# Optimization experiments

Measured on AMD Instinct MI355X. Metric: run time of the kernel, lower is better.

Reference implementation:

```python
import jax, jax.numpy as jnp
import numpy as np

NGRAM = 4
PAD = 0
N_LAYERS = sum(range(1, NGRAM + 1)) - 1  # 9; blocks_size = 10


def setup_inputs() -> dict:
    B, L, D, V = 8, 2048, 256, 256
    rng = np.random.default_rng(0)
    lens = rng.integers(L // 2, L + 1, size=B)
    pos = np.arange(L)
    seq = rng.integers(1, V, size=(B, L))
    seq = np.where(pos[None, :] < lens[:, None], seq, PAD)
    # per-layer block sizes: (size,offset) combos of GBST, sizes [2,2,3,3,3,4,4,4,4]
    sizes = [n for n in range(1, NGRAM + 1) for _ in range(n)][1:]
    gid = np.zeros((B, N_LAYERS, L), dtype=np.int64)
    for li, s in enumerate(sizes):
        g = pos // s + 1  # sorted contiguous group ids starting at 1
        gid[:, li, :] = np.where(pos[None, :] < lens[:, None], g[None, :], PAD)

    key = jax.random.key(0)
    ks = jax.random.split(key, 8)
    emb = jax.random.normal(ks[0], (V, D), jnp.float32) * 0.02
    conv_w = jax.random.normal(ks[1], (D, 1, NGRAM), jnp.float32) * 0.3      # depthwise Conv1d weight [out,1,k]
    conv_b = jax.random.normal(ks[2], (D,), jnp.float32) * 0.01
    proj_w = jax.random.normal(ks[3], (D, D), jnp.float32) / np.sqrt(D)      # 1x1 conv as [out,in]
    proj_b = jax.random.normal(ks[4], (D,), jnp.float32) * 0.01
    score_w = jax.random.normal(ks[5], (D,), jnp.float32) / np.sqrt(D)       # Linear(D,1)
    score_b = jnp.zeros((), jnp.float32)
    ff_w = jax.random.normal(ks[6], (D, D), jnp.float32) / np.sqrt(D)        # Linear(D,D) weight [out,in]
    ff_b = jax.random.normal(ks[7], (D,), jnp.float32) * 0.01
    return {
        "sequence": jnp.asarray(seq, jnp.int64) if jax.config.jax_enable_x64 else jnp.asarray(seq, jnp.int32),
        "group_id": jnp.asarray(gid, jnp.int64) if jax.config.jax_enable_x64 else jnp.asarray(gid, jnp.int32),
        "emb": emb, "conv_w": conv_w, "conv_b": conv_b,
        "proj_w": proj_w, "proj_b": proj_b,
        "score_w": score_w, "score_b": score_b,
        "ff_w": ff_w, "ff_b": ff_b,
    }


def _pool_one(xb, gb):
    """Per-(batch,layer) scatter_mean + broadcast back. xb:[L,D], gb:[L]."""
    L = gb.shape[0]
    mask = gb == PAD
    xm = jnp.where(mask[:, None], 0.0, xb)          # zero padded positions
    pad_g = jnp.max(gb) + 1                         # pad positions -> extra trailing group
    g = jnp.where(mask, pad_g, gb) - 1              # 0-based group ids
    sums = jax.ops.segment_sum(xm, g, num_segments=L)
    cnts = jax.ops.segment_sum(jnp.ones((L,), xb.dtype), g, num_segments=L)
    means = sums / jnp.maximum(cnts, 1.0)[:, None]
    # group ids are sorted-contiguous, so repeat_interleave(bincount) == gather
    return means[g]


def reference(sequence, group_id, emb, conv_w, conv_b, proj_w, proj_b,
              score_w, score_b, ff_w, ff_b):
    B, L = sequence.shape
    D = emb.shape[1]
    # NormalizedEmbedding: lookup * sqrt(d_model)
    x = emb[sequence] * jnp.sqrt(jnp.asarray(D, emb.dtype))          # [B,L,D]
    xp = jnp.pad(x, ((0, 0), (0, NGRAM - 1), (0, 0)))                # pad seq end
    xc = xp.transpose(0, 2, 1)                                       # [B,D,L+k-1]
    xc = jax.lax.conv_general_dilated(
        xc, conv_w, window_strides=(1,), padding='VALID',
        feature_group_count=D, dimension_numbers=('NCH', 'OIH', 'NCH'))
    xc = xc + conv_b[None, :, None]
    xc = jnp.einsum('ed,bdl->bel', proj_w, xc) + proj_b[None, :, None]
    x = xc.transpose(0, 2, 1)                                        # [B,L,D]
    seq_mask = sequence == PAD
    x = jnp.where(seq_mask[..., None], 0.0, x)

    # layers 1..9 are computed on a detached copy in the original
    xd = jax.lax.stop_gradient(x)
    pooled = jax.vmap(jax.vmap(_pool_one, in_axes=(None, 0)),
                      in_axes=(0, 0))(xd, group_id)                  # [B,9,L,D]

    block_reps = jnp.concatenate([x[:, None], pooled], axis=1)       # [B,10,L,D]
    block_reps = block_reps.transpose(0, 2, 1, 3)                    # [B,L,10,D]

    scores = jnp.einsum('blsd,d->bls', block_reps, score_w) + score_b
    blocks_mask = jnp.concatenate([sequence[:, None], group_id], axis=1)
    blocks_mask = blocks_mask.transpose(0, 2, 1) == PAD              # [B,L,10]
    neg = -jnp.finfo(scores.dtype).max
    scores = jnp.where(blocks_mask, neg, scores)
    scores = jax.nn.softmax(scores, axis=2)

    out = jnp.einsum('blsd,bls->bld', block_reps, scores)            # [B,L,D]
    out = out + jax.nn.relu(out @ ff_w.T + ff_b)
    return out
```

## Files before the change

kernel.cpp:

```cpp
#include <hip/hip_runtime.h>
#include <math.h>


#define D_ 256
#define M_ 24
#define BPB 86
#define LSTR 264

typedef __attribute__((ext_vector_type(8))) short bf16x8;
typedef __attribute__((ext_vector_type(4))) float f32x4;

__device__ __forceinline__ ushort f2bf(float f) {
    union { float f; unsigned u; } v; v.f = f;
    unsigned r = v.u + 0x7fffu + ((v.u >> 16) & 1u);
    return (ushort)(r >> 16);
}
__device__ __forceinline__ float bf2f(ushort h) {
    union { unsigned u; float f; } v; v.u = ((unsigned)h) << 16;
    return v.f;
}

#define LDB4(v0, v1, v2, v3, W, K8) do { \
    const ushort* bp_ = (W) + ((size_t)((K8) * 16 + w * 4) * 64 + ln) * 8; \
    v0 = *(const bf16x8*)(bp_); \
    v1 = *(const bf16x8*)(bp_ + 512); \
    v2 = *(const bf16x8*)(bp_ + 1024); \
    v3 = *(const bf16x8*)(bp_ + 1536); \
} while (0)

#define MFMA8(ACC, K8, v0, v1, v2, v3) do { \
    bf16x8 a0_ = *(const bf16x8*)&x_lds[lr][(K8) * 32 + koff]; \
    bf16x8 a1_ = *(const bf16x8*)&x_lds[16 + lr][(K8) * 32 + koff]; \
    ACC[0][0] = __builtin_amdgcn_mfma_f32_16x16x32_bf16(a0_, v0, ACC[0][0], 0, 0, 0); \
    ACC[1][0] = __builtin_amdgcn_mfma_f32_16x16x32_bf16(a1_, v0, ACC[1][0], 0, 0, 0); \
    ACC[0][1] = __builtin_amdgcn_mfma_f32_16x16x32_bf16(a0_, v1, ACC[0][1], 0, 0, 0); \
    ACC[1][1] = __builtin_amdgcn_mfma_f32_16x16x32_bf16(a1_, v1, ACC[1][1], 0, 0, 0); \
    ACC[0][2] = __builtin_amdgcn_mfma_f32_16x16x32_bf16(a0_, v2, ACC[0][2], 0, 0, 0); \
    ACC[1][2] = __builtin_amdgcn_mfma_f32_16x16x32_bf16(a1_, v2, ACC[1][2], 0, 0, 0); \
    ACC[0][3] = __builtin_amdgcn_mfma_f32_16x16x32_bf16(a0_, v3, ACC[0][3], 0, 0, 0); \
    ACC[1][3] = __builtin_amdgcn_mfma_f32_16x16x32_bf16(a1_, v3, ACC[1][3], 0, 0, 0); \
} while (0)

#define SBAR __builtin_amdgcn_sched_barrier(0)

__global__ __launch_bounds__(256) void k_prep(
    const float* __restrict__ pw, const float* __restrict__ fw,
    const float* __restrict__ emb,
    ushort* __restrict__ wqp, ushort* __restrict__ wqf, ushort* __restrict__ we)
{
    int i = blockIdx.x * 256 + threadIdx.x;
    we[i] = f2bf(emb[i] * 16.0f);
    int j  = i & 7;
    int ln = (i >> 3) & 63;
    int nb = (i >> 9) & 15;
    int k8 = i >> 13;
    int er = nb * 16 + (ln & 15);
    int k  = k8 * 32 + (ln >> 4) * 8 + j;
    wqp[i] = f2bf(pw[er * D_ + k]);
    wqf[i] = f2bf(fw[er * D_ + k]);
}

__global__ __launch_bounds__(256, 3) void k_main(
    const int* __restrict__ seq, const ushort* __restrict__ we,
    const float* __restrict__ conv_w, const float* __restrict__ conv_b,
    const ushort* __restrict__ wqp, const float* __restrict__ proj_b,
    const float* __restrict__ score_w,
    const ushort* __restrict__ wqf, const float* __restrict__ ff_b,
    float* __restrict__ out, int L)
{
    __shared__ ushort x_lds[32][LSTR];
    __shared__ ushort x2[M_][LSTR];
    __shared__ float xsred[4][M_];
    __shared__ float wts[4][12][4];
    __shared__ int sseq[4][M_ + 3];
    const int b  = blockIdx.x / BPB;
    const int l0 = (blockIdx.x % BPB) * M_;
    const int t  = threadIdx.x;
    const int w  = t >> 6, ln = t & 63;
    const int lr = ln & 15, q = ln >> 4;
    const int koff = q * 8;

    if (ln < M_ + 3) {
        int l = l0 + ln;
        sseq[w][ln] = (l < L) ? seq[b * L + l] : -1;
    }
    {
        int zr = 24 + (t >> 5), zc = (t & 31) * 8;
        *(uint4*)&x_lds[zr][zc] = make_uint4(0, 0, 0, 0);
    }
    bf16x8 s00, s01, s02, s03, s10, s11, s12, s13;
    bf16x8 s20, s21, s22, s23, s30, s31, s32, s33;
    LDB4(s00, s01, s02, s03, wqp, 0);
    LDB4(s10, s11, s12, s13, wqp, 1);
    LDB4(s20, s21, s22, s23, wqp, 2);
    LDB4(s30, s31, s32, s33, wqp, 3);
    SBAR;
    asm volatile("s_waitcnt lgkmcnt(0)" ::: "memory");
    SBAR;

    {
        const int h = t >> 7;
        const int ch0 = (t & 127) * 2;
        float2 er[15];
        #pragma unroll
        for (int r = 0; r < 15; ++r) {
            int sn = sseq[w][h * 12 + r];
            float ex = 0.f, ey = 0.f;
            if (sn >= 0) {
                unsigned v = *(const unsigned*)(we + sn * D_ + ch0);
                ex = bf2f((ushort)(v & 0xffff));
                ey = bf2f((ushort)(v >> 16));
            }
            er[r].x = ex; er[r].y = ey;
        }
        const float4 wa = *(const float4*)(conv_w + ch0 * 4);
        const float4 wb = *(const float4*)(conv_w + ch0 * 4 + 4);
        const float cba = conv_b[ch0], cbb = conv_b[ch0 + 1];
        #pragma unroll
        for (int r = 0; r < 12; ++r) {
            float cx = fmaf(wa.x, er[r].x, fmaf(wa.y, er[r+1].x,
                       fmaf(wa.z, er[r+2].x, fmaf(wa.w, er[r+3].x, cba))));
            float cy = fmaf(wb.x, er[r].y, fmaf(wb.y, er[r+1].y,
                       fmaf(wb.z, er[r+2].y, fmaf(wb.w, er[r+3].y, cbb))));
            *(unsigned*)&x_lds[h * 12 + r][ch0] =
                (unsigned)f2bf(cx) | ((unsigned)f2bf(cy) << 16);
        }
    }
    __syncthreads();

    f32x4 acc[2][4];
    #pragma unroll
    for (int s = 0; s < 2; ++s)
        #pragma unroll
        for (int n = 0; n < 4; ++n) acc[s][n] = (f32x4){0.f, 0.f, 0.f, 0.f};
    MFMA8(acc, 0, s00, s01, s02, s03); LDB4(s00, s01, s02, s03, wqp, 4); SBAR;
    MFMA8(acc, 1, s10, s11, s12, s13); LDB4(s10, s11, s12, s13, wqp, 5); SBAR;
    MFMA8(acc, 2, s20, s21, s22, s23); LDB4(s20, s21, s22, s23, wqp, 6); SBAR;
    MFMA8(acc, 3, s30, s31, s32, s33); LDB4(s30, s31, s32, s33, wqp, 7); SBAR;
    MFMA8(acc, 4, s00, s01, s02, s03);
    MFMA8(acc, 5, s10, s11, s12, s13);
    MFMA8(acc, 6, s20, s21, s22, s23);
    MFMA8(acc, 7, s30, s31, s32, s33);

    {
        float xsp[8] = {0,0,0,0,0,0,0,0};
        #pragma unroll
        for (int n = 0; n < 4; ++n) {
            int e = w * 64 + n * 16 + lr;
            float pb = proj_b[e], sw = score_w[e];
            #pragma unroll
            for (int s = 0; s < 2; ++s) {
                #pragma unroll
                for (int r = 0; r < 4; ++r) {
                    int row = s * 16 + q * 4 + r;
                    if (row < M_) {
                        float v = (sseq[w][row] > 0) ? acc[s][n][r] + pb : 0.f;
                        x2[row][e] = f2bf(v);
                        xsp[s * 4 + r] = fmaf(v, sw, xsp[s * 4 + r]);
                    }
                }
            }
        }
        #pragma unroll
        for (int off = 1; off < 16; off <<= 1) {
            #pragma unroll
            for (int i = 0; i < 8; ++i) xsp[i] += __shfl_xor(xsp[i], off, 64);
        }
        if (lr == 0) {
            #pragma unroll
            for (int r = 0; r < 4; ++r) xsred[w][q * 4 + r] = xsp[r];
            if (q < 2) {
                #pragma unroll
                for (int r = 0; r < 4; ++r) xsred[w][16 + q * 4 + r] = xsp[4 + r];
            }
        }
    }
    __syncthreads();

    LDB4(s00, s01, s02, s03, wqf, 0);
    LDB4(s10, s11, s12, s13, wqf, 1);
    LDB4(s20, s21, s22, s23, wqf, 2);
    LDB4(s30, s31, s32, s33, wqf, 3);
    SBAR;

    if (ln < 12) {
        const int p = (w >> 1) * 12 + ln;
        if (sseq[w][p] <= 0) {
            wts[w][ln][0] = wts[w][ln][1] = wts[w][ln][2] = wts[w][ln][3] = 0.f;
        } else {
            #define XS(i) (xsred[0][i] + xsred[1][i] + xsred[2][i] + xsred[3][i])
            #define FL(i) ((sseq[w][i] > 0) ? 1.f : 0.f)
            float s0 = XS(p);
            int r2 = p & ~1;
            float c2 = fmaxf(FL(r2) + FL(r2+1), 1.f);
            float m2 = (XS(r2) + XS(r2+1)) / c2;
            int r3 = p - (p % 3);
            float c3 = fmaxf(FL(r3) + FL(r3+1) + FL(r3+2), 1.f);
            float m3 = (XS(r3) + XS(r3+1) + XS(r3+2)) / c3;
            int r4 = p & ~3;
            float c4 = fmaxf(FL(r4) + FL(r4+1) + FL(r4+2) + FL(r4+3), 1.f);
            float m4 = (XS(r4) + XS(r4+1) + XS(r4+2) + XS(r4+3)) / c4;
            float mx = fmaxf(fmaxf(s0, m2), fmaxf(m3, m4));
            float q0 = expf(s0 - mx), q2 = expf(m2 - mx);
            float q3 = expf(m3 - mx), q4 = expf(m4 - mx);
            float iZ = 1.f / (q0 + 2.f * q2 + 3.f * q3 + 4.f * q4);
            wts[w][ln][0] = q0 * iZ;
            wts[w][ln][1] = 2.f * q2 * iZ / c2;
            wts[w][ln][2] = 3.f * q3 * iZ / c3;
            wts[w][ln][3] = 4.f * q4 * iZ / c4;
            #undef XS
            #undef FL
        }
    }
    asm volatile("s_waitcnt lgkmcnt(0)" ::: "memory");
    SBAR;

    {
        const int tile = t >> 7;
        const int r0 = tile * 12;
        const int ch0 = (t & 127) * 2;
        float2 xr[12];
        #pragma unroll
        for (int p = 0; p < 12; ++p) {
            unsigned v = *(const unsigned*)&x2[r0 + p][ch0];
            xr[p].x = bf2f((ushort)(v & 0xffff));
            xr[p].y = bf2f((ushort)(v >> 16));
        }
        float s2x[6], s2y[6], s3x[4], s3y[4], s4x[3], s4y[3];
        #pragma unroll
        for (int j = 0; j < 6; ++j) {
            s2x[j] = xr[2*j].x + xr[2*j+1].x;
            s2y[j] = xr[2*j].y + xr[2*j+1].y;
        }
        #pragma unroll
        for (int j = 0; j < 4; ++j) {
            s3x[j] = xr[3*j].x + xr[3*j+1].x + xr[3*j+2].x;
            s3y[j] = xr[3*j].y + xr[3*j+1].y + xr[3*j+2].y;
        }
        #pragma unroll
        for (int j = 0; j < 3; ++j) {
            s4x[j] = xr[4*j].x + xr[4*j+1].x + xr[4*j+2].x + xr[4*j+3].x;
            s4y[j] = xr[4*j].y + xr[4*j+1].y + xr[4*j+2].y + xr[4*j+3].y;
        }
        #pragma unroll
        for (int p = 0; p < 12; ++p) {
            float4 wv = *(const float4*)&wts[w][p][0];
            float ox = wv.x*xr[p].x + wv.y*s2x[p>>1] + wv.z*s3x[p/3] + wv.w*s4x[p>>2];
            float oy = wv.x*xr[p].y + wv.y*s2y[p>>1] + wv.z*s3y[p/3] + wv.w*s4y[p>>2];
            *(unsigned*)&x_lds[r0 + p][ch0] =
                (unsigned)f2bf(ox) | ((unsigned)f2bf(oy) << 16);
        }
    }
    __syncthreads();

    f32x4 ffa[2][4];
    #pragma unroll
    for (int s = 0; s < 2; ++s)
        #pragma unroll
        for (int n = 0; n < 4; ++n) ffa[s][n] = (f32x4){0.f, 0.f, 0.f, 0.f};
    MFMA8(ffa, 0, s00, s01, s02, s03); LDB4(s00, s01, s02, s03, wqf, 4); SBAR;
    MFMA8(ffa, 1, s10, s11, s12, s13); LDB4(s10, s11, s12, s13, wqf, 5); SBAR;
    MFMA8(ffa, 2, s20, s21, s22, s23); LDB4(s20, s21, s22, s23, wqf, 6); SBAR;
    MFMA8(ffa, 3, s30, s31, s32, s33); LDB4(s30, s31, s32, s33, wqf, 7); SBAR;
    MFMA8(ffa, 4, s00, s01, s02, s03);
    MFMA8(ffa, 5, s10, s11, s12, s13);
    MFMA8(ffa, 6, s20, s21, s22, s23);
    MFMA8(ffa, 7, s30, s31, s32, s33);

    #pragma unroll
    for (int n = 0; n < 4; ++n) {
        int e = w * 64 + n * 16 + lr;
        float fb = ff_b[e];
        #pragma unroll
        for (int s = 0; s < 2; ++s) {
            #pragma unroll
            for (int r = 0; r < 4; ++r) {
                int row = s * 16 + q * 4 + r;
                if (row < M_) {
                    int l = l0 + row;
                    if (l < L) {
                        float o = bf2f(x_lds[row][e]);
                        out[((size_t)b * L + l) * D_ + e]
                            = o + fmaxf(ffa[s][n][r] + fb, 0.f);
                    }
                }
            }
        }
    }
}

extern "C" void kernel_launch(void* const* d_in, const int* in_sizes, int n_in,
                              void* d_out, int out_size, void* d_ws, size_t ws_size,
                              hipStream_t stream) {
    const int*   seq     = (const int*)d_in[0];
    const float* emb     = (const float*)d_in[2];
    const float* conv_w  = (const float*)d_in[3];
    const float* conv_b  = (const float*)d_in[4];
    const float* proj_w  = (const float*)d_in[5];
    const float* proj_b  = (const float*)d_in[6];
    const float* score_w = (const float*)d_in[7];
    const float* ff_w    = (const float*)d_in[9];
    const float* ff_b    = (const float*)d_in[10];
    float* out = (float*)d_out;

    const int L = 2048;
    const int B = in_sizes[0] / L;

    ushort* wqp = (ushort*)d_ws;
    ushort* wqf = wqp + D_ * D_;
    ushort* we  = wqf + D_ * D_;

    k_prep<<<D_ * D_ / 256, 256, 0, stream>>>(proj_w, ff_w, emb, wqp, wqf, we);
    k_main<<<B * BPB, 256, 0, stream>>>(seq, we, conv_w, conv_b, wqp, proj_b,
                                        score_w, wqf, ff_b, out, L);
}
```

Before: 30.31 us.

## Read fp32 embeddings directly, keep tokens in scalar registers, shrink weight prefetch for occupancy

```diff
diff --git a/kernel.cpp b/kernel.cpp
--- a/kernel.cpp
+++ b/kernel.cpp
@@ -45,11 +45,9 @@
 
 __global__ __launch_bounds__(256) void k_prep(
     const float* __restrict__ pw, const float* __restrict__ fw,
-    const float* __restrict__ emb,
-    ushort* __restrict__ wqp, ushort* __restrict__ wqf, ushort* __restrict__ we)
+    ushort* __restrict__ wqp, ushort* __restrict__ wqf)
 {
     int i = blockIdx.x * 256 + threadIdx.x;
-    we[i] = f2bf(emb[i] * 16.0f);
     int j  = i & 7;
     int ln = (i >> 3) & 63;
     int nb = (i >> 9) & 15;
@@ -60,8 +58,8 @@
     wqf[i] = f2bf(fw[er * D_ + k]);
 }
 
-__global__ __launch_bounds__(256, 3) void k_main(
-    const int* __restrict__ seq, const ushort* __restrict__ we,
+__global__ __launch_bounds__(256, 4) void k_main(
+    const int* __restrict__ seq, const float* __restrict__ emb,
     const float* __restrict__ conv_w, const float* __restrict__ conv_b,
     const ushort* __restrict__ wqp, const float* __restrict__ proj_b,
     const float* __restrict__ score_w,
@@ -72,7 +70,6 @@
     __shared__ ushort x2[M_][LSTR];
     __shared__ float xsred[4][M_];
     __shared__ float wts[4][12][4];
-    __shared__ int sseq[4][M_ + 3];
     const int b  = blockIdx.x / BPB;
     const int l0 = (blockIdx.x % BPB) * M_;
     const int t  = threadIdx.x;
@@ -80,51 +77,60 @@
     const int lr = ln & 15, q = ln >> 4;
     const int koff = q * 8;
 
-    if (ln < M_ + 3) {
-        int l = l0 + ln;
-        sseq[w][ln] = (l < L) ? seq[b * L + l] : -1;
-    }
-    {
-        int zr = 24 + (t >> 5), zc = (t & 31) * 8;
-        *(uint4*)&x_lds[zr][zc] = make_uint4(0, 0, 0, 0);
-    }
-    bf16x8 s00, s01, s02, s03, s10, s11, s12, s13;
-    bf16x8 s20, s21, s22, s23, s30, s31, s32, s33;
+    int tok[M_ + 3];
+    {
+        const int* seqp = seq + (size_t)b * L + l0;
+        #pragma unroll
+        for (int r = 0; r < M_ + 3; ++r) {
+            int tv = -1;
+            if (l0 + r < L) tv = __builtin_amdgcn_readfirstlane(seqp[r]);
+            tok[r] = tv;
+        }
+    }
+    unsigned vmask = 0;
+    #pragma unroll
+    for (int r = 0; r < M_; ++r) vmask |= (tok[r] > 0) ? (1u << r) : 0u;
+
+    bf16x8 s00, s01, s02, s03, s10, s11, s12, s13, s20, s21, s22, s23;
     LDB4(s00, s01, s02, s03, wqp, 0);
     LDB4(s10, s11, s12, s13, wqp, 1);
     LDB4(s20, s21, s22, s23, wqp, 2);
-    LDB4(s30, s31, s32, s33, wqp, 3);
     SBAR;
-    asm volatile("s_waitcnt lgkmcnt(0)" ::: "memory");
-    SBAR;
+
+    {
+        int zr = 24 + (t >> 5), zc = (t & 31) * 8;
+        *(uint4*)&x_lds[zr][zc] = make_uint4(0, 0, 0, 0);
+    }
 
     {
         const int h = t >> 7;
         const int ch0 = (t & 127) * 2;
-        float2 er[15];
-        #pragma unroll
-        for (int r = 0; r < 15; ++r) {
-            int sn = sseq[w][h * 12 + r];
-            float ex = 0.f, ey = 0.f;
-            if (sn >= 0) {
-                unsigned v = *(const unsigned*)(we + sn * D_ + ch0);
-                ex = bf2f((ushort)(v & 0xffff));
-                ey = bf2f((ushort)(v >> 16));
-            }
-            er[r].x = ex; er[r].y = ey;
-        }
-        const float4 wa = *(const float4*)(conv_w + ch0 * 4);
-        const float4 wb = *(const float4*)(conv_w + ch0 * 4 + 4);
+        float4 wa = *(const float4*)(conv_w + ch0 * 4);
+        float4 wb = *(const float4*)(conv_w + ch0 * 4 + 4);
+        wa.x *= 16.f; wa.y *= 16.f; wa.z *= 16.f; wa.w *= 16.f;
+        wb.x *= 16.f; wb.y *= 16.f; wb.z *= 16.f; wb.w *= 16.f;
         const float cba = conv_b[ch0], cbb = conv_b[ch0 + 1];
-        #pragma unroll
-        for (int r = 0; r < 12; ++r) {
-            float cx = fmaf(wa.x, er[r].x, fmaf(wa.y, er[r+1].x,
-                       fmaf(wa.z, er[r+2].x, fmaf(wa.w, er[r+3].x, cba))));
-            float cy = fmaf(wb.x, er[r].y, fmaf(wb.y, er[r+1].y,
-                       fmaf(wb.z, er[r+2].y, fmaf(wb.w, er[r+3].y, cbb))));
-            *(unsigned*)&x_lds[h * 12 + r][ch0] =
-                (unsigned)f2bf(cx) | ((unsigned)f2bf(cy) << 16);
-        }
+        #define CONV_HALF(BASE) do { \
+            float2 er[15]; \
+            _Pragma("unroll") \
+            for (int r = 0; r < 15; ++r) { \
+                int sn = tok[(BASE) + r]; \
+                float2 e; e.x = 0.f; e.y = 0.f; \
+                if (sn >= 0) e = *(const float2*)(emb + (size_t)sn * D_ + ch0); \
+                er[r] = e; \
+            } \
+            _Pragma("unroll") \
+            for (int r = 0; r < 12; ++r) { \
+                float cx = fmaf(wa.x, er[r].x, fmaf(wa.y, er[r+1].x, \
+                           fmaf(wa.z, er[r+2].x, fmaf(wa.w, er[r+3].x, cba)))); \
+                float cy = fmaf(wb.x, er[r].y, fmaf(wb.y, er[r+1].y, \
+                           fmaf(wb.z, er[r+2].y, fmaf(wb.w, er[r+3].y, cbb)))); \
+                *(unsigned*)&x_lds[(BASE) + r][ch0] = \
+                    (unsigned)f2bf(cx) | ((unsigned)f2bf(cy) << 16); \
+            } \
+        } while (0)
+        if (h == 0) { CONV_HALF(0); } else { CONV_HALF(12); }
+        #undef CONV_HALF
     }
     __syncthreads();
 
@@ -133,14 +139,14 @@
     for (int s = 0; s < 2; ++s)
         #pragma unroll
         for (int n = 0; n < 4; ++n) acc[s][n] = (f32x4){0.f, 0.f, 0.f, 0.f};
-    MFMA8(acc, 0, s00, s01, s02, s03); LDB4(s00, s01, s02, s03, wqp, 4); SBAR;
-    MFMA8(acc, 1, s10, s11, s12, s13); LDB4(s10, s11, s12, s13, wqp, 5); SBAR;
-    MFMA8(acc, 2, s20, s21, s22, s23); LDB4(s20, s21, s22, s23, wqp, 6); SBAR;
-    MFMA8(acc, 3, s30, s31, s32, s33); LDB4(s30, s31, s32, s33, wqp, 7); SBAR;
-    MFMA8(acc, 4, s00, s01, s02, s03);
-    MFMA8(acc, 5, s10, s11, s12, s13);
-    MFMA8(acc, 6, s20, s21, s22, s23);
-    MFMA8(acc, 7, s30, s31, s32, s33);
+    MFMA8(acc, 0, s00, s01, s02, s03); LDB4(s00, s01, s02, s03, wqp, 3); SBAR;
+    MFMA8(acc, 1, s10, s11, s12, s13); LDB4(s10, s11, s12, s13, wqp, 4); SBAR;
+    MFMA8(acc, 2, s20, s21, s22, s23); LDB4(s20, s21, s22, s23, wqp, 5); SBAR;
+    MFMA8(acc, 3, s00, s01, s02, s03); LDB4(s00, s01, s02, s03, wqp, 6); SBAR;
+    MFMA8(acc, 4, s10, s11, s12, s13); LDB4(s10, s11, s12, s13, wqp, 7); SBAR;
+    MFMA8(acc, 5, s20, s21, s22, s23);
+    MFMA8(acc, 6, s00, s01, s02, s03);
+    MFMA8(acc, 7, s10, s11, s12, s13);
 
     {
         float xsp[8] = {0,0,0,0,0,0,0,0};
@@ -154,7 +160,7 @@
                 for (int r = 0; r < 4; ++r) {
                     int row = s * 16 + q * 4 + r;
                     if (row < M_) {
-                        float v = (sseq[w][row] > 0) ? acc[s][n][r] + pb : 0.f;
+                        float v = ((vmask >> row) & 1u) ? acc[s][n][r] + pb : 0.f;
                         x2[row][e] = f2bf(v);
                         xsp[s * 4 + r] = fmaf(v, sw, xsp[s * 4 + r]);
                     }
@@ -180,36 +186,33 @@
     LDB4(s00, s01, s02, s03, wqf, 0);
     LDB4(s10, s11, s12, s13, wqf, 1);
     LDB4(s20, s21, s22, s23, wqf, 2);
-    LDB4(s30, s31, s32, s33, wqf, 3);
     SBAR;
 
     if (ln < 12) {
         const int p = (w >> 1) * 12 + ln;
-        if (sseq[w][p] <= 0) {
+        if (!((vmask >> p) & 1u)) {
             wts[w][ln][0] = wts[w][ln][1] = wts[w][ln][2] = wts[w][ln][3] = 0.f;
         } else {
             #define XS(i) (xsred[0][i] + xsred[1][i] + xsred[2][i] + xsred[3][i])
-            #define FL(i) ((sseq[w][i] > 0) ? 1.f : 0.f)
             float s0 = XS(p);
             int r2 = p & ~1;
-            float c2 = fmaxf(FL(r2) + FL(r2+1), 1.f);
-            float m2 = (XS(r2) + XS(r2+1)) / c2;
+            float c2 = (float)__popc((vmask >> r2) & 3u);
+            float m2 = (XS(r2) + XS(r2 + 1)) / c2;
             int r3 = p - (p % 3);
-            float c3 = fmaxf(FL(r3) + FL(r3+1) + FL(r3+2), 1.f);
-            float m3 = (XS(r3) + XS(r3+1) + XS(r3+2)) / c3;
+            float c3 = (float)__popc((vmask >> r3) & 7u);
+            float m3 = (XS(r3) + XS(r3 + 1) + XS(r3 + 2)) / c3;
             int r4 = p & ~3;
-            float c4 = fmaxf(FL(r4) + FL(r4+1) + FL(r4+2) + FL(r4+3), 1.f);
-            float m4 = (XS(r4) + XS(r4+1) + XS(r4+2) + XS(r4+3)) / c4;
+            float c4 = (float)__popc((vmask >> r4) & 15u);
+            float m4 = (XS(r4) + XS(r4 + 1) + XS(r4 + 2) + XS(r4 + 3)) / c4;
             float mx = fmaxf(fmaxf(s0, m2), fmaxf(m3, m4));
-            float q0 = expf(s0 - mx), q2 = expf(m2 - mx);
-            float q3 = expf(m3 - mx), q4 = expf(m4 - mx);
+            float q0 = __expf(s0 - mx), q2 = __expf(m2 - mx);
+            float q3 = __expf(m3 - mx), q4 = __expf(m4 - mx);
             float iZ = 1.f / (q0 + 2.f * q2 + 3.f * q3 + 4.f * q4);
             wts[w][ln][0] = q0 * iZ;
             wts[w][ln][1] = 2.f * q2 * iZ / c2;
             wts[w][ln][2] = 3.f * q3 * iZ / c3;
             wts[w][ln][3] = 4.f * q4 * iZ / c4;
             #undef XS
-            #undef FL
         }
     }
     asm volatile("s_waitcnt lgkmcnt(0)" ::: "memory");
@@ -258,14 +261,14 @@
     for (int s = 0; s < 2; ++s)
         #pragma unroll
         for (int n = 0; n < 4; ++n) ffa[s][n] = (f32x4){0.f, 0.f, 0.f, 0.f};
-    MFMA8(ffa, 0, s00, s01, s02, s03); LDB4(s00, s01, s02, s03, wqf, 4); SBAR;
-    MFMA8(ffa, 1, s10, s11, s12, s13); LDB4(s10, s11, s12, s13, wqf, 5); SBAR;
-    MFMA8(ffa, 2, s20, s21, s22, s23); LDB4(s20, s21, s22, s23, wqf, 6); SBAR;
-    MFMA8(ffa, 3, s30, s31, s32, s33); LDB4(s30, s31, s32, s33, wqf, 7); SBAR;
-    MFMA8(ffa, 4, s00, s01, s02, s03);
-    MFMA8(ffa, 5, s10, s11, s12, s13);
-    MFMA8(ffa, 6, s20, s21, s22, s23);
-    MFMA8(ffa, 7, s30, s31, s32, s33);
+    MFMA8(ffa, 0, s00, s01, s02, s03); LDB4(s00, s01, s02, s03, wqf, 3); SBAR;
+    MFMA8(ffa, 1, s10, s11, s12, s13); LDB4(s10, s11, s12, s13, wqf, 4); SBAR;
+    MFMA8(ffa, 2, s20, s21, s22, s23); LDB4(s20, s21, s22, s23, wqf, 5); SBAR;
+    MFMA8(ffa, 3, s00, s01, s02, s03); LDB4(s00, s01, s02, s03, wqf, 6); SBAR;
+    MFMA8(ffa, 4, s10, s11, s12, s13); LDB4(s10, s11, s12, s13, wqf, 7); SBAR;
+    MFMA8(ffa, 5, s20, s21, s22, s23);
+    MFMA8(ffa, 6, s00, s01, s02, s03);
+    MFMA8(ffa, 7, s10, s11, s12, s13);
 
     #pragma unroll
     for (int n = 0; n < 4; ++n) {
@@ -308,9 +311,8 @@
 
     ushort* wqp = (ushort*)d_ws;
     ushort* wqf = wqp + D_ * D_;
-    ushort* we  = wqf + D_ * D_;
-
-    k_prep<<<D_ * D_ / 256, 256, 0, stream>>>(proj_w, ff_w, emb, wqp, wqf, we);
-    k_main<<<B * BPB, 256, 0, stream>>>(seq, we, conv_w, conv_b, wqp, proj_b,
+
+    k_prep<<<D_ * D_ / 256, 256, 0, stream>>>(proj_w, ff_w, wqp, wqf);
+    k_main<<<B * BPB, 256, 0, stream>>>(seq, emb, conv_w, conv_b, wqp, proj_b,
                                         score_w, wqf, ff_b, out, L);
 }
```

Measured after the change: 28.53 us. 1.06x faster.
